# Kernel optimization log

Hardware: AMD Instinct MI355X
Metric: run time of the kernel (lower is better)

The kernel has to match this reference:

```python
import jax, jax.numpy as jnp
import numpy as np

H = 1024      # lstm_hidden_size
LABELS = 122  # slot label size


def setup_inputs() -> dict:
    key = jax.random.key(0)
    ks = jax.random.split(key, 8)
    s_in = 1.0 / np.sqrt(5 * H)
    s_h = 1.0 / np.sqrt(H)
    return {
        "x": jax.random.normal(ks[0], (1, 512, 2 * H), jnp.float32),
        "hi": jax.random.normal(ks[1], (1, 512, 2 * H), jnp.float32),
        # LSTM params (PyTorch layout: gates ordered i, f, g, o)
        "W_ih": jax.random.uniform(ks[2], (4 * H, 5 * H), jnp.float32, -s_in, s_in),
        "W_hh": jax.random.uniform(ks[3], (4 * H, H), jnp.float32, -s_h, s_h),
        "b_ih": jax.random.uniform(ks[4], (4 * H,), jnp.float32, -s_h, s_h),
        "b_hh": jax.random.uniform(ks[5], (4 * H,), jnp.float32, -s_h, s_h),
        "W_fc": jax.random.uniform(ks[6], (LABELS, H), jnp.float32, -s_h, s_h),
        "b_fc": jax.random.uniform(ks[7], (LABELS,), jnp.float32, -s_h, s_h),
    }


def _decode(x, hi, W_ih, W_hh, b_ih, b_hh, W_fc, b_fc):
    # x, hi: [1, L, 2H] -> per-step encoder features [L, 4H] (batch fixed at 1)
    feats = jnp.concatenate([x, hi], axis=-1)[0]
    bias = b_ih + b_hh

    def step(carry, f_t):
        h, c, prev_out = carry
        z = jnp.concatenate([f_t, prev_out])              # [5H]: cat(x_t, hi_t, out_{t-1})
        gates = W_ih @ z + W_hh @ h + bias                # [4H]
        i, f, g, o = jnp.split(gates, 4)
        c_new = jax.nn.sigmoid(f) * c + jax.nn.sigmoid(i) * jnp.tanh(g)
        h_new = jax.nn.sigmoid(o) * jnp.tanh(c_new)
        return (h_new, c_new, h_new), h_new

    zero = jnp.zeros((H,), x.dtype)
    _, outs = jax.lax.scan(step, (zero, zero, zero), feats)  # outs: [L, H]
    res = outs @ W_fc.T + b_fc                               # [L, LABELS]
    return res[None]                                         # [1, L, LABELS]


def reference(x, hi, W_ih, W_hh, b_ih, b_hh, W_fc, b_fc):
    return _decode(x, hi, W_ih, W_hh, b_ih, b_hh, W_fc, b_fc)
```

## Files before the change

kernel.cpp:

```cpp
#include <hip/hip_runtime.h>
#include <hip/hip_fp16.h>
#include <math.h>

#define HD    1024
#define SEQL  512
#define NLAB  122
#define NWG   128
#define TPW   512
#define JPW   8

#define OFF_MSG   ((size_t)0)
#define OFF_HALL  ((size_t)16384)
#define OFF_GATES ((size_t)2113536)
#define OFF_WR    ((size_t)10502144)
#define OFF_W1H   ((size_t)27279360)
#define OFF_FH    ((size_t)60833792)
#define WS_NEED   ((size_t)65028096)

typedef unsigned long long u64;
typedef _Float16 v8h __attribute__((ext_vector_type(8)));
typedef float v4f __attribute__((ext_vector_type(4)));
typedef float v2f __attribute__((ext_vector_type(2)));
typedef unsigned int v4u __attribute__((ext_vector_type(4)));

__global__ __launch_bounds__(256) void prep_wr(const float* __restrict__ W_ih,
                                               const float* __restrict__ W_hh,
                                               float* __restrict__ W_r2) {
    int o = blockIdx.x * 256 + threadIdx.x;
    int g   = o >> 13;
    int i   = (o >> 9) & 15;
    int t   = o & 511;
    int row = t & 31;
    int kq  = t >> 5;
    int gate = row >> 3;
    int jj   = row & 7;
    int R = (gate << 10) + (g << 3) + jj;
    int k = (kq << 6) + (i << 2);
    float4 wa = *(const float4*)(W_ih + (size_t)R * 5120 + 4096 + k);
    float4 wb = *(const float4*)(W_hh + (size_t)R * 1024 + k);
    float4 out;
    out.x = wa.x + wb.x; out.y = wa.y + wb.y; out.z = wa.z + wb.z; out.w = wa.w + wb.w;
    *(float4*)(W_r2 + (size_t)o * 4) = out;
}

static __device__ __forceinline__ uint4 pack8(float4 f0, float4 f1) {
    __half2 p0 = __floats2half2_rn(f0.x, f0.y);
    __half2 p1 = __floats2half2_rn(f0.z, f0.w);
    __half2 p2 = __floats2half2_rn(f1.x, f1.y);
    __half2 p3 = __floats2half2_rn(f1.z, f1.w);
    uint4 o;
    o.x = *(unsigned*)&p0; o.y = *(unsigned*)&p1;
    o.z = *(unsigned*)&p2; o.w = *(unsigned*)&p3;
    return o;
}

__global__ __launch_bounds__(256) void prep_fh(const float* __restrict__ x,
                                               const float* __restrict__ hi,
                                               uint4* __restrict__ F_h) {
    int o = blockIdx.x * 256 + threadIdx.x;
    int t = o >> 9;
    int u = o & 511;
    const float* src = (u < 256) ? (x  + (size_t)t * 2048 + u * 8)
                                 : (hi + (size_t)t * 2048 + (u - 256) * 8);
    F_h[o] = pack8(*(const float4*)src, *(const float4*)(src + 4));
}

__global__ __launch_bounds__(256) void prep_w1h(const float* __restrict__ W_ih,
                                                uint4* __restrict__ W1h) {
    int o = blockIdx.x * 256 + threadIdx.x;
    int r = o >> 9;
    int u = o & 511;
    const float* src = W_ih + (size_t)r * 5120 + u * 8;
    W1h[o] = pack8(*(const float4*)src, *(const float4*)(src + 4));
}

__global__ __launch_bounds__(256) void gates_mfma(const uint4* __restrict__ F_u4,
                                                  const uint4* __restrict__ W_u4,
                                                  const float* __restrict__ b_ih,
                                                  const float* __restrict__ b_hh,
                                                  float* __restrict__ gates_x) {
    __shared__ uint4 AsB[1024];
    const _Float16* Ash = (const _Float16*)AsB;
    const _Float16* Bsh = Ash + 4096;
    const int tid  = threadIdx.x;
    const int wv   = tid >> 6;
    const int lane = tid & 63;
    const int wr   = wv & 1;
    const int wc   = wv >> 1;
    const int n0 = blockIdx.x * 128;
    const int t0 = blockIdx.y * 128;

    const int u0 = tid * 2, u1 = tid * 2 + 1;
    const uint4* aSrc0 = F_u4 + (size_t)(t0 + (u0 >> 2)) * 512 + (u0 & 3);
    const uint4* aSrc1 = F_u4 + (size_t)(t0 + (u1 >> 2)) * 512 + (u1 & 3);
    const uint4* bSrc0 = W_u4 + (size_t)(n0 + (u0 >> 2)) * 512 + (u0 & 3);
    const uint4* bSrc1 = W_u4 + (size_t)(n0 + (u1 >> 2)) * 512 + (u1 & 3);

    v4f acc[4][4];
    #pragma unroll
    for (int mi = 0; mi < 4; ++mi)
        #pragma unroll
        for (int ni = 0; ni < 4; ++ni)
            acc[mi][ni] = (v4f){0.f, 0.f, 0.f, 0.f};

    const int aoff = (wr * 64 + (lane & 15)) * 32 + (lane >> 4) * 8;
    const int boff = (wc * 64 + (lane & 15)) * 32 + (lane >> 4) * 8;

    for (int it = 0; it < 128; ++it) {
        uint4 a0 = aSrc0[it * 4], a1 = aSrc1[it * 4];
        uint4 b0 = bSrc0[it * 4], b1 = bSrc1[it * 4];
        __syncthreads();
        AsB[u0]       = a0; AsB[u1]       = a1;
        AsB[512 + u0] = b0; AsB[512 + u1] = b1;
        __syncthreads();
        v8h a8[4], b8[4];
        #pragma unroll
        for (int mi = 0; mi < 4; ++mi)
            a8[mi] = *(const v8h*)(Ash + aoff + mi * 16 * 32);
        #pragma unroll
        for (int ni = 0; ni < 4; ++ni)
            b8[ni] = *(const v8h*)(Bsh + boff + ni * 16 * 32);
        #pragma unroll
        for (int mi = 0; mi < 4; ++mi)
            #pragma unroll
            for (int ni = 0; ni < 4; ++ni)
                acc[mi][ni] = __builtin_amdgcn_mfma_f32_16x16x32_f16(
                                  a8[mi], b8[ni], acc[mi][ni], 0, 0, 0);
    }

    #pragma unroll
    for (int ni = 0; ni < 4; ++ni) {
        int r = n0 + wc * 64 + ni * 16 + (lane & 15);
        int sidx = ((r & 1023) >> 3) * 32 + (r >> 10) * 8 + (r & 7);
        float bias = b_ih[r] + b_hh[r];
        #pragma unroll
        for (int mi = 0; mi < 4; ++mi) {
            int tb = t0 + wr * 64 + mi * 16 + ((lane >> 4) << 2);
            #pragma unroll
            for (int reg = 0; reg < 4; ++reg)
                gates_x[(size_t)(tb + reg) * 4096 + sidx] = acc[mi][ni][reg] + bias;
        }
    }
}

__global__ __launch_bounds__(256) void gates_gemm_f32(const float* __restrict__ x,
                                                      const float* __restrict__ hi,
                                                      const float* __restrict__ W_ih,
                                                      const float* __restrict__ b_ih,
                                                      const float* __restrict__ b_hh,
                                                      float* __restrict__ gates_x) {
    __shared__ float As[16][68];
    __shared__ float Bs[16][68];
    const int tid = threadIdx.x;
    const int r0 = blockIdx.x * 64;
    const int t0 = blockIdx.y * 64;
    const int tx = tid & 15, ty = tid >> 4;
    const int l   = tid & 63;
    const int kq4 = tid >> 6;

    float acc[4][4] = {};
    for (int kb = 0; kb < 4096; kb += 16) {
        int k = kb + kq4 * 4;
        const float* asrc = (k < 2048) ? (x  + (size_t)(t0 + l) * 2048 + k)
                                       : (hi + (size_t)(t0 + l) * 2048 + (k - 2048));
        float4 a4 = *(const float4*)asrc;
        float4 b4 = *(const float4*)(W_ih + (size_t)(r0 + l) * 5120 + k);
        __syncthreads();
        As[kq4 * 4 + 0][l] = a4.x; As[kq4 * 4 + 1][l] = a4.y;
        As[kq4 * 4 + 2][l] = a4.z; As[kq4 * 4 + 3][l] = a4.w;
        Bs[kq4 * 4 + 0][l] = b4.x; Bs[kq4 * 4 + 1][l] = b4.y;
        Bs[kq4 * 4 + 2][l] = b4.z; Bs[kq4 * 4 + 3][l] = b4.w;
        __syncthreads();
        #pragma unroll
        for (int kk = 0; kk < 16; ++kk) {
            float4 av = *(const float4*)&As[kk][ty * 4];
            float4 bv = *(const float4*)&Bs[kk][tx * 4];
            float a_[4] = {av.x, av.y, av.z, av.w};
            float b_[4] = {bv.x, bv.y, bv.z, bv.w};
            #pragma unroll
            for (int i = 0; i < 4; ++i)
                #pragma unroll
                for (int j = 0; j < 4; ++j)
                    acc[i][j] += a_[i] * b_[j];
        }
    }
    int r = r0 + tx * 4;
    float bias[4];
    #pragma unroll
    for (int j = 0; j < 4; ++j) bias[j] = b_ih[r + j] + b_hh[r + j];
    int gate = r >> 10;
    int g    = (r & 1023) >> 3;
    int jj   = r & 7;
    int sidx = g * 32 + gate * 8 + jj;
    #pragma unroll
    for (int i = 0; i < 4; ++i) {
        float4 o;
        o.x = acc[i][0] + bias[0]; o.y = acc[i][1] + bias[1];
        o.z = acc[i][2] + bias[2]; o.w = acc[i][3] + bias[3];
        *(float4*)(gates_x + (size_t)(t0 + ty * 4 + i) * 4096 + sidx) = o;
    }
}

__global__ __launch_bounds__(512, 1) void lstm_rec(const float* __restrict__ gates_x,
                                                   const float* __restrict__ W_r2,
                                                   float* __restrict__ h_all,
                                                   u64* h_msg) {
    const int g   = blockIdx.x;
    const int tid = threadIdx.x;
    const int row = tid & 31;
    const int kq  = tid >> 5;
    __shared__ float4 W_lds[16][TPW];
    __shared__ float4 h_s4[256];
    __shared__ float  partial[8][36];
    float* h_sf = (float*)h_s4;

    {
        const float4* Wp = (const float4*)W_r2 + (size_t)g * 8192;
        #pragma unroll
        for (int i = 0; i < 16; ++i)
            W_lds[i][tid] = Wp[i * TPW + tid];
    }
    __syncthreads();

    float c = 0.f;
    int budget = 4000000;

    for (int s = 0; s < SEQL; ++s) {
        asm volatile("" ::: "memory");
        float4 w[16];
        #pragma unroll
        for (int i = 0; i < 16; ++i)
            w[i] = W_lds[i][tid];
        asm volatile("" ::: "memory");

        {
            const u64 addr = (u64)(h_msg + (size_t)(s & 1) * HD + tid * 2);
            const unsigned want = (unsigned)s;
            v4u r0, r1, rr;
            asm volatile(
                "global_load_dwordx4 %0, %2, off sc1\n\t"
                "global_load_dwordx4 %1, %2, off sc1"
                : "=&v"(r0), "=&v"(r1) : "v"(addr) : "memory");
            for (;;) {
                asm volatile("s_waitcnt vmcnt(1)" ::: "memory");
                __builtin_amdgcn_sched_barrier(0);
                if ((r0.y == want && r0.w == want) | (--budget < 0)) { rr = r0; break; }
                asm volatile("global_load_dwordx4 %0, %1, off sc1"
                             : "=&v"(r0) : "v"(addr) : "memory");
                asm volatile("s_waitcnt vmcnt(1)" ::: "memory");
                __builtin_amdgcn_sched_barrier(0);
                if ((r1.y == want && r1.w == want) | (--budget < 0)) { rr = r1; break; }
                asm volatile("global_load_dwordx4 %0, %1, off sc1"
                             : "=&v"(r1) : "v"(addr) : "memory");
            }
            asm volatile("s_waitcnt vmcnt(0)" ::: "memory");
            __builtin_amdgcn_sched_barrier(0);
            asm volatile("" :: "v"(r0), "v"(r1));
            ((v2f*)h_sf)[tid] = (v2f){__uint_as_float(rr.x), __uint_as_float(rr.z)};
        }
        asm volatile("" ::: "memory");

        float gx = 0.f;
        if (tid < 32)
            gx = gates_x[(size_t)s * 4096 + g * 32 + tid];

        float a0 = 0.f, a1 = 0.f, a2 = 0.f, a3 = 0.f;
        #pragma unroll
        for (int i = 0; i < 16; ++i) {
            float4 h4 = h_s4[kq * 16 + i];
            a0 += w[i].x * h4.x;
            a1 += w[i].y * h4.y;
            a2 += w[i].z * h4.z;
            a3 += w[i].w * h4.w;
        }
        float p = (a0 + a1) + (a2 + a3);
        p += __shfl_xor(p, 32, 64);
        if ((tid & 32) == 0)
            partial[tid >> 6][row] = p;
        __syncthreads();

        if (tid < 32) {
            float sum = gx;
            #pragma unroll
            for (int q = 0; q < 8; ++q) sum += partial[q][tid];
            bool isg = ((tid >> 3) == 2);
            float e   = __expf(isg ? -2.f * sum : -sum);
            float act = isg ? (2.f / (1.f + e) - 1.f) : (1.f / (1.f + e));
            int jj = tid & 7;
            float sf = __shfl(act,  8 + jj, 64);
            float tg = __shfl(act, 16 + jj, 64);
            float so = __shfl(act, 24 + jj, 64);
            if (tid < 8) {
                float si = act;
                c = sf * c + si * tg;
                float th = 2.f / (1.f + __expf(-2.f * c)) - 1.f;
                float h = so * th;
                int j = g * JPW + tid;
                h_all[(size_t)s * HD + j] = h;
                u64 m = ((u64)(unsigned)(s + 1) << 32)
                      | (u64)__float_as_uint(h);
                __hip_atomic_store(h_msg + (size_t)((s + 1) & 1) * HD + j, m,
                                   __ATOMIC_RELAXED, __HIP_MEMORY_SCOPE_AGENT);
            }
        }
    }
}

__global__ __launch_bounds__(128) void fc_out(const float* __restrict__ h_all,
                                              const float* __restrict__ W_fc,
                                              const float* __restrict__ b_fc,
                                              float* __restrict__ out) {
    const int t0 = blockIdx.x * 4;
    const int tid = threadIdx.x;
    __shared__ float4 h_s[1024];
    const float4* hsrc = (const float4*)(h_all + (size_t)t0 * HD);
    #pragma unroll
    for (int i = 0; i < 8; ++i)
        h_s[tid + i * 128] = hsrc[tid + i * 128];
    __syncthreads();
    if (tid < NLAB) {
        float b = b_fc[tid];
        float acc0 = b, acc1 = b, acc2 = b, acc3 = b;
        const float4* wp = (const float4*)(W_fc + (size_t)tid * HD);
        #pragma unroll 4
        for (int k4 = 0; k4 < 256; ++k4) {
            float4 w = wp[k4];
            float4 h0 = h_s[k4];
            float4 h1 = h_s[256 + k4];
            float4 h2 = h_s[512 + k4];
            float4 h3 = h_s[768 + k4];
            acc0 += w.x*h0.x + w.y*h0.y + w.z*h0.z + w.w*h0.w;
            acc1 += w.x*h1.x + w.y*h1.y + w.z*h1.z + w.w*h1.w;
            acc2 += w.x*h2.x + w.y*h2.y + w.z*h2.z + w.w*h2.w;
            acc3 += w.x*h3.x + w.y*h3.y + w.z*h3.z + w.w*h3.w;
        }
        out[(size_t)(t0 + 0) * NLAB + tid] = acc0;
        out[(size_t)(t0 + 1) * NLAB + tid] = acc1;
        out[(size_t)(t0 + 2) * NLAB + tid] = acc2;
        out[(size_t)(t0 + 3) * NLAB + tid] = acc3;
    }
}

extern "C" void kernel_launch(void* const* d_in, const int* in_sizes, int n_in,
                              void* d_out, int out_size, void* d_ws, size_t ws_size,
                              hipStream_t stream) {
    const float* x    = (const float*)d_in[0];
    const float* hi   = (const float*)d_in[1];
    const float* W_ih = (const float*)d_in[2];
    const float* W_hh = (const float*)d_in[3];
    const float* b_ih = (const float*)d_in[4];
    const float* b_hh = (const float*)d_in[5];
    const float* W_fc = (const float*)d_in[6];
    const float* b_fc = (const float*)d_in[7];
    float* out = (float*)d_out;

    char* ws = (char*)d_ws;
    u64*   h_msg   = (u64*)(ws + OFF_MSG);
    float* h_all   = (float*)(ws + OFF_HALL);
    float* gates_x = (float*)(ws + OFF_GATES);
    float* W_r2    = (float*)(ws + OFF_WR);
    uint4* W1h     = (uint4*)(ws + OFF_W1H);
    uint4* F_h     = (uint4*)(ws + OFF_FH);

    hipMemsetAsync(d_ws, 0, 16384, stream);

    prep_wr<<<4096, 256, 0, stream>>>(W_ih, W_hh, W_r2);

    if (ws_size >= WS_NEED) {
        prep_fh<<<1024, 256, 0, stream>>>(x, hi, F_h);
        prep_w1h<<<8192, 256, 0, stream>>>(W_ih, W1h);
        dim3 gg(32, 4);
        gates_mfma<<<gg, 256, 0, stream>>>(F_h, W1h, b_ih, b_hh, gates_x);
    } else {
        dim3 gg(64, 8);
        gates_gemm_f32<<<gg, 256, 0, stream>>>(x, hi, W_ih, b_ih, b_hh, gates_x);
    }

    lstm_rec<<<NWG, TPW, 0, stream>>>(gates_x, W_r2, h_all, h_msg);

    fc_out<<<SEQL / 4, 128, 0, stream>>>(h_all, W_fc, b_fc, out);
}
```

Baseline: 1.341 ms.

## Replicate h broadcast buffer across workgroup groups to spread polling traffic

After: 1.243 ms. 7.4% less time.

```diff
diff --git a/kernel.cpp b/kernel.cpp
--- a/kernel.cpp
+++ b/kernel.cpp
@@ -16,6 +16,9 @@
 #define OFF_W1H   ((size_t)27279360)
 #define OFF_FH    ((size_t)60833792)
 #define WS_NEED   ((size_t)65028096)
+#define REP_MAX   8
+#define OFF_MSG8  WS_NEED
+#define WS_NEED8  (WS_NEED + (size_t)2 * REP_MAX * HD * 8)
 
 typedef unsigned long long u64;
 typedef _Float16 v8h __attribute__((ext_vector_type(8)));
@@ -204,11 +207,12 @@
 __global__ __launch_bounds__(512, 1) void lstm_rec(const float* __restrict__ gates_x,
                                                    const float* __restrict__ W_r2,
                                                    float* __restrict__ h_all,
-                                                   u64* h_msg) {
+                                                   u64* h_msg, int rep) {
     const int g   = blockIdx.x;
     const int tid = threadIdx.x;
     const int row = tid & 31;
     const int kq  = tid >> 5;
+    const int cp  = g & (rep - 1);
     __shared__ float4 W_lds[16][TPW];
     __shared__ float4 h_s4[256];
     __shared__ float  partial[8][36];
@@ -226,6 +230,10 @@
     int budget = 4000000;
 
     for (int s = 0; s < SEQL; ++s) {
+        float gx = 0.f;
+        if (tid < 32)
+            gx = gates_x[(size_t)s * 4096 + g * 32 + tid];
+
         asm volatile("" ::: "memory");
         float4 w[16];
         #pragma unroll
@@ -234,35 +242,23 @@
         asm volatile("" ::: "memory");
 
         {
-            const u64 addr = (u64)(h_msg + (size_t)(s & 1) * HD + tid * 2);
+            const u64 addr = (u64)(h_msg +
+                                   ((size_t)((s & 1) * rep + cp)) * HD + tid * 2);
             const unsigned want = (unsigned)s;
-            v4u r0, r1, rr;
-            asm volatile(
-                "global_load_dwordx4 %0, %2, off sc1\n\t"
-                "global_load_dwordx4 %1, %2, off sc1"
-                : "=&v"(r0), "=&v"(r1) : "v"(addr) : "memory");
+            v4u ra;
             for (;;) {
-                asm volatile("s_waitcnt vmcnt(1)" ::: "memory");
-                __builtin_amdgcn_sched_barrier(0);
-                if ((r0.y == want && r0.w == want) | (--budget < 0)) { rr = r0; break; }
-                asm volatile("global_load_dwordx4 %0, %1, off sc1"
-                             : "=&v"(r0) : "v"(addr) : "memory");
-                asm volatile("s_waitcnt vmcnt(1)" ::: "memory");
-                __builtin_amdgcn_sched_barrier(0);
-                if ((r1.y == want && r1.w == want) | (--budget < 0)) { rr = r1; break; }
-                asm volatile("global_load_dwordx4 %0, %1, off sc1"
-                             : "=&v"(r1) : "v"(addr) : "memory");
+                asm volatile(
+                    "global_load_dwordx4 %0, %1, off sc1\n\t"
+                    "s_waitcnt vmcnt(0)"
+                    : "=&v"(ra)
+                    : "v"(addr)
+                    : "memory");
+                if (ra.y == want && ra.w == want) break;
+                if (--budget < 0) break;
             }
-            asm volatile("s_waitcnt vmcnt(0)" ::: "memory");
-            __builtin_amdgcn_sched_barrier(0);
-            asm volatile("" :: "v"(r0), "v"(r1));
-            ((v2f*)h_sf)[tid] = (v2f){__uint_as_float(rr.x), __uint_as_float(rr.z)};
+            ((v2f*)h_sf)[tid] = (v2f){__uint_as_float(ra.x), __uint_as_float(ra.z)};
         }
         asm volatile("" ::: "memory");
-
-        float gx = 0.f;
-        if (tid < 32)
-            gx = gates_x[(size_t)s * 4096 + g * 32 + tid];
 
         float a0 = 0.f, a1 = 0.f, a2 = 0.f, a3 = 0.f;
         #pragma unroll
@@ -299,8 +295,10 @@
                 h_all[(size_t)s * HD + j] = h;
                 u64 m = ((u64)(unsigned)(s + 1) << 32)
                       | (u64)__float_as_uint(h);
-                __hip_atomic_store(h_msg + (size_t)((s + 1) & 1) * HD + j, m,
-                                   __ATOMIC_RELAXED, __HIP_MEMORY_SCOPE_AGENT);
+                u64* dst = h_msg + (size_t)(((s + 1) & 1) * rep) * HD + j;
+                for (int r = 0; r < rep; ++r)
+                    __hip_atomic_store(dst + (size_t)r * HD, m,
+                                       __ATOMIC_RELAXED, __HIP_MEMORY_SCOPE_AGENT);
             }
         }
     }
@@ -355,14 +353,23 @@
     float* out = (float*)d_out;
 
     char* ws = (char*)d_ws;
-    u64*   h_msg   = (u64*)(ws + OFF_MSG);
     float* h_all   = (float*)(ws + OFF_HALL);
     float* gates_x = (float*)(ws + OFF_GATES);
     float* W_r2    = (float*)(ws + OFF_WR);
     uint4* W1h     = (uint4*)(ws + OFF_W1H);
     uint4* F_h     = (uint4*)(ws + OFF_FH);
 
-    hipMemsetAsync(d_ws, 0, 16384, stream);
+    u64* h_msg;
+    int  rep;
+    if (ws_size >= WS_NEED8) {
+        h_msg = (u64*)(ws + OFF_MSG8);
+        rep   = REP_MAX;
+        hipMemsetAsync(h_msg, 0, (size_t)2 * REP_MAX * HD * 8, stream);
+    } else {
+        h_msg = (u64*)(ws + OFF_MSG);
+        rep   = 1;
+        hipMemsetAsync(h_msg, 0, 16384, stream);
+    }
 
     prep_wr<<<4096, 256, 0, stream>>>(W_ih, W_hh, W_r2);
 
@@ -376,7 +383,7 @@
         gates_gemm_f32<<<gg, 256, 0, stream>>>(x, hi, W_ih, b_ih, b_hh, gates_x);
     }
 
-    lstm_rec<<<NWG, TPW, 0, stream>>>(gates_x, W_r2, h_all, h_msg);
+    lstm_rec<<<NWG, TPW, 0, stream>>>(gates_x, W_r2, h_all, h_msg, rep);
 
     fc_out<<<SEQL / 4, 128, 0, stream>>>(h_all, W_fc, b_fc, out);
 }
```
